# Kernel tuning notes

Hardware: AMD Instinct MI355X
Metric: run time of the kernel (lower is better)

The kernel has to match this reference:

```python
import math
import jax, jax.numpy as jnp
import numpy as np

B, S, E, H = 2, 2048, 1024, 16
Dh = E // H  # 64
ROPE_BASE = 10000.0


def setup_inputs() -> dict:
    key = jax.random.key(0)
    ks = jax.random.split(key, 7)
    f32 = jnp.float32
    return {
        "q": jax.random.normal(ks[0], (B, S, E), dtype=f32),
        "k": jax.random.normal(ks[1], (B, S, E), dtype=f32),
        "v": jax.random.normal(ks[2], (B, S, E), dtype=f32),
        # nn.Linear weights stored torch-style as [out_features, in_features]
        "W_q": jax.random.normal(ks[3], (E, E), dtype=f32) * 0.02,
        "W_k": jax.random.normal(ks[4], (E, E), dtype=f32) * 0.02,
        "W_v": jax.random.normal(ks[5], (E, E), dtype=f32) * 0.02,
        "W_o": jax.random.normal(ks[6], (E, E), dtype=f32) * 0.02,
    }


def _rope(x):
    # x: [B, H, S, Dh]; interleaved-pair rotary embedding along the seq axis.
    d = x.shape[-1]
    pos = jnp.arange(x.shape[2], dtype=x.dtype)
    inv_freq = 1.0 / (ROPE_BASE ** (jnp.arange(0, d, 2, dtype=x.dtype) / d))
    ang = pos[:, None] * inv_freq            # [S, Dh//2]
    cos, sin = jnp.cos(ang), jnp.sin(ang)    # broadcast over [B, H]
    xe, xo = x[..., 0::2], x[..., 1::2]      # even/odd interleaved pairs
    out = jnp.stack([xe * cos - xo * sin, xo * cos + xe * sin], axis=-1)
    return out.reshape(x.shape)


def reference(q, k, v, W_q, W_k, W_v, W_o):
    b, s, e = q.shape
    scale = 1.0 / math.sqrt(e)  # NOTE: 1/sqrt(hidden_dim), not head_dim (faithful)
    # project and split heads: [B, H, S, Dh]
    qh = (q @ W_q.T).reshape(b, s, H, Dh).transpose(0, 2, 1, 3)
    kh = (k @ W_k.T).reshape(b, s, H, Dh).transpose(0, 2, 1, 3)
    vh = (v @ W_v.T).reshape(b, s, H, Dh).transpose(0, 2, 1, 3)
    qh = _rope(qh)
    kh = _rope(kh)
    scores = jnp.einsum('bhsd,bhtd->bhst', qh, kh) * scale
    # Faithful quirk: the original sets causal_mask[0,0] = False, which zeroes
    # the ENTIRE [S,S] mask (dims 0,1 are singletons) -> masked_fill is a no-op.
    probs = jax.nn.softmax(scores, axis=-1)
    out = jnp.einsum('bhst,bhtd->bhsd', probs, vh)
    out = out.transpose(0, 2, 1, 3).reshape(b, s, e)
    return out @ W_o.T
```

## Files before the change

kernel.cpp:

```cpp
#include <hip/hip_runtime.h>
#include <math.h>

#define Bsz 2
#define Ssz 2048
#define Esz 1024
#define Hn  16
#define Dd  64
#define PADC 72

typedef unsigned short ushort_t;
typedef short bf16x8 __attribute__((ext_vector_type(8)));
typedef float f32x4 __attribute__((ext_vector_type(4)));

#define GLD16(g, l) __builtin_amdgcn_global_load_lds(                        \
    (const __attribute__((address_space(1))) unsigned int*)(g),              \
    (__attribute__((address_space(3))) unsigned int*)(l), 16, 0, 0)

__global__ __launch_bounds__(256) void rope_table_kernel(float* tc, float* ts)
{
    const int idx = blockIdx.x * 256 + threadIdx.x;
    const int s = idx >> 5, p = idx & 31;
    const double c = 9.210340371976184257 / 32.0;
    const double inv = exp(-c * (double)p);
    double sn, cs;
    sincos((double)s * inv, &sn, &cs);
    tc[idx] = (float)cs;
    ts[idx] = (float)sn;
}

__device__ inline ushort_t bf16_rn(float x)
{
    unsigned u = __float_as_uint(x);
    return (ushort_t)((u + 0x7FFFu + ((u >> 16) & 1u)) >> 16);
}

__device__ inline void bsplit(float x, ushort_t& h, ushort_t& l)
{
    unsigned u = __float_as_uint(x);
    unsigned hr = (u + 0x7FFFu + ((u >> 16) & 1u)) >> 16;
    h = (ushort_t)hr;
    float lo = x - __uint_as_float(hr << 16);
    l = bf16_rn(lo);
}

__global__ __launch_bounds__(256) void cvt_kernel(
    const float* s0, const float* s1, const float* s2,
    const float* s3, const float* s4, const float* s5,
    ushort_t* d0, ushort_t* d1, ushort_t* d2,
    ushort_t* d3, ushort_t* d4, ushort_t* d5, int n_big, int n_small)
{
    const float* s; ushort_t* d;
    switch (blockIdx.z) {
        case 0: s = s0; d = d0; break;
        case 1: s = s1; d = d1; break;
        case 2: s = s2; d = d2; break;
        case 3: s = s3; d = d3; break;
        case 4: s = s4; d = d4; break;
        default: s = s5; d = d5; break;
    }
    const int n = (blockIdx.z < 3) ? n_big : n_small;
    const int i = (blockIdx.x * 256 + threadIdx.x) * 4;
    if (i >= n) return;
    float4 v = *(const float4*)(s + i);
    ushort4 o;
    o.x = bf16_rn(v.x); o.y = bf16_rn(v.y);
    o.z = bf16_rn(v.z); o.w = bf16_rn(v.w);
    *(ushort4*)(d + i) = o;
}

__global__ __launch_bounds__(256) void wsplit_kernel(
    const float* s, ushort_t* ph, ushort_t* pl, int n)
{
    const int i = (blockIdx.x * 256 + threadIdx.x) * 4;
    if (i >= n) return;
    float4 v = *(const float4*)(s + i);
    ushort4 hv, lv;
    bsplit(v.x, hv.x, lv.x);
    bsplit(v.y, hv.y, lv.y);
    bsplit(v.z, hv.z, lv.z);
    bsplit(v.w, hv.w, lv.w);
    *(ushort4*)(ph + i) = hv;
    *(ushort4*)(pl + i) = lv;
}

__global__ __launch_bounds__(256) void proj_gemm_kernel(
    const ushort_t* __restrict__ Aq, const ushort_t* __restrict__ Ak,
    const ushort_t* __restrict__ Av,
    const ushort_t* __restrict__ Wq, const ushort_t* __restrict__ Wk,
    const ushort_t* __restrict__ Wv,
    ushort_t* __restrict__ Yq, ushort_t* __restrict__ Yk,
    ushort_t* __restrict__ Yv,
    const float* __restrict__ tc, const float* __restrict__ ts)
{
    const int z = blockIdx.z;
    const ushort_t* Ag = (z == 0) ? Aq : (z == 1) ? Ak : Av;
    const ushort_t* Wg = (z == 0) ? Wq : (z == 1) ? Wk : Wv;
    ushort_t*       Yg = (z == 0) ? Yq : (z == 1) ? Yk : Yv;
    const bool rope = (z < 2);

    __shared__ __align__(16) ushort_t sA[128 * 32];
    __shared__ __align__(16) ushort_t sB[64 * 32];

    const int t    = threadIdx.x;
    const int lane = t & 63;
    const int wv   = t >> 6;
    const int wm   = (wv & 1) * 64;
    const int wn   = (wv >> 1) * 32;
    const int fr   = lane & 15;
    const int kq   = (lane >> 4) * 8;
    const int n0   = blockIdx.x * 64;
    const int m0   = blockIdx.y * 128;

    const ushort_t* pA = Ag + (size_t)(m0 + (t >> 2)) * 1024 + (t & 3) * 8;
    const ushort_t* pB = Wg + (size_t)(n0 + (t >> 2)) * 1024 + (t & 3) * 8;

    f32x4 acc[4][2];
#pragma unroll
    for (int mi = 0; mi < 4; ++mi)
#pragma unroll
        for (int ni = 0; ni < 2; ++ni) acc[mi][ni] = (f32x4)0.f;

    for (int k0 = 0; k0 < 1024; k0 += 32) {
        GLD16(pA + k0,             &sA[t * 8]);
        GLD16(pA + k0 + 64 * 1024, &sA[2048 + t * 8]);
        GLD16(pB + k0,             &sB[t * 8]);
        __syncthreads();

        bf16x8 a[4], b[2];
#pragma unroll
        for (int mi = 0; mi < 4; ++mi)
            a[mi] = *(const bf16x8*)&sA[(wm + mi * 16 + fr) * 32 + kq];
#pragma unroll
        for (int ni = 0; ni < 2; ++ni)
            b[ni] = *(const bf16x8*)&sB[(wn + ni * 16 + fr) * 32 + kq];
#pragma unroll
        for (int mi = 0; mi < 4; ++mi)
#pragma unroll
            for (int ni = 0; ni < 2; ++ni)
                acc[mi][ni] = __builtin_amdgcn_mfma_f32_16x16x32_bf16(
                    a[mi], b[ni], acc[mi][ni], 0, 0, 0);
        __syncthreads();
    }

#pragma unroll
    for (int mi = 0; mi < 4; ++mi)
#pragma unroll
        for (int ni = 0; ni < 2; ++ni) {
            const int col   = n0 + wn + ni * 16 + fr;
            const int rbase = m0 + wm + mi * 16 + (lane >> 4) * 4;
            const int hh = col >> 6, d = col & 63, pi = d >> 1;
#pragma unroll
            for (int rg = 0; rg < 4; ++rg) {
                const int srow = rbase + rg;
                const int b_ = srow >> 11, s = srow & (Ssz - 1);
                float v  = acc[mi][ni][rg];
                float pt = __shfl_xor(v, 1, 64);
                float o  = v;
                if (rope) {
                    const float cs = tc[s * 32 + pi];
                    const float sn = ts[s * 32 + pi];
                    o = (d & 1) ? fmaf(v, cs, pt * sn)
                                : fmaf(v, cs, -pt * sn);
                }
                const size_t idx = (z == 2)
                    ? (((size_t)(b_ * Hn + hh)) * Dd + d) * Ssz + s
                    : (((size_t)(b_ * Hn + hh)) * Ssz + s) * Dd + d;
                Yg[idx] = bf16_rn(o);
            }
        }
}

__global__ __launch_bounds__(256) void attn_bf16_kernel(
    const ushort_t* __restrict__ Qb, const ushort_t* __restrict__ Kb,
    const ushort_t* __restrict__ Vtb,
    ushort_t* __restrict__ Oh, ushort_t* __restrict__ Ol)
{
    __shared__ __align__(16) ushort_t sK[64 * PADC];
    __shared__ __align__(16) ushort_t sV[64 * PADC];
    __shared__ __align__(16) ushort_t sP[64 * PADC];

    const int t    = threadIdx.x;
    const int lane = t & 63;
    const int w    = t >> 6;
    const int fr   = lane & 15;
    const int g    = lane >> 4;
    const int kq   = g * 8;
    const int bh   = blockIdx.y;
    const int q0   = blockIdx.x * 64;

    const size_t qbase = ((size_t)bh * Ssz + q0 + w * 16 + fr) * Dd;
    bf16x8 qa[2];
    qa[0] = *(const bf16x8*)(Qb + qbase + kq);
    qa[1] = *(const bf16x8*)(Qb + qbase + 32 + kq);

    float lp[4];
    f32x4 Oacc[4];
#pragma unroll
    for (int r = 0; r < 4; ++r) lp[r] = 0.f;
#pragma unroll
    for (int dt = 0; dt < 4; ++dt) Oacc[dt] = (f32x4)0.f;

    const int srow = t >> 3;
    const int scol = (t & 7) * 8;
    const size_t kgb = (size_t)bh * Ssz * Dd;
    const size_t vgb = (size_t)bh * Dd * Ssz;

    const float kf = 0.045084220027780106f;

    for (int kv0 = 0; kv0 < Ssz; kv0 += 64) {
#pragma unroll
        for (int rr = 0; rr < 2; ++rr) {
            const int row = srow + rr * 32;
            *(uint4*)&sK[row * PADC + scol] =
                *(const uint4*)(Kb + kgb + (size_t)(kv0 + row) * Dd + scol);
            *(uint4*)&sV[row * PADC + scol] =
                *(const uint4*)(Vtb + vgb + (size_t)row * Ssz + kv0 + scol);
        }
        __syncthreads();

        f32x4 S[4];
#pragma unroll
        for (int nt = 0; nt < 4; ++nt) S[nt] = (f32x4)0.f;
#pragma unroll
        for (int ks = 0; ks < 2; ++ks)
#pragma unroll
            for (int nt = 0; nt < 4; ++nt) {
                bf16x8 kf_ = *(const bf16x8*)&sK[(nt * 16 + fr) * PADC + ks * 32 + kq];
                S[nt] = __builtin_amdgcn_mfma_f32_16x16x32_bf16(qa[ks], kf_, S[nt], 0, 0, 0);
            }

#pragma unroll
        for (int nt = 0; nt < 4; ++nt)
#pragma unroll
            for (int rg = 0; rg < 4; ++rg) {
                const float p = exp2f(S[nt][rg] * kf);
                lp[rg] += p;
                sP[(w * 16 + g * 4 + rg) * PADC + nt * 16 + fr] = bf16_rn(p);
            }
        __syncthreads();

#pragma unroll
        for (int ks = 0; ks < 2; ++ks) {
            bf16x8 pa = *(const bf16x8*)&sP[(w * 16 + fr) * PADC + ks * 32 + kq];
#pragma unroll
            for (int dt = 0; dt < 4; ++dt) {
                bf16x8 vf = *(const bf16x8*)&sV[(dt * 16 + fr) * PADC + ks * 32 + kq];
                Oacc[dt] = __builtin_amdgcn_mfma_f32_16x16x32_bf16(pa, vf, Oacc[dt], 0, 0, 0);
            }
        }
        __syncthreads();
    }

#pragma unroll
    for (int rg = 0; rg < 4; ++rg) {
#pragma unroll
        for (int mk = 1; mk <= 8; mk <<= 1)
            lp[rg] += __shfl_xor(lp[rg], mk, 64);
    }

    const int b = bh >> 4, h = bh & 15;
#pragma unroll
    for (int rg = 0; rg < 4; ++rg) {
        const int s = q0 + w * 16 + g * 4 + rg;
        const float inv = 1.f / lp[rg];
#pragma unroll
        for (int dt = 0; dt < 4; ++dt) {
            const float o = Oacc[dt][rg] * inv;
            ushort_t oh, ol;
            bsplit(o, oh, ol);
            const size_t idx = ((size_t)(b * Ssz + s)) * Esz + h * Dd + dt * 16 + fr;
            Oh[idx] = oh;
            Ol[idx] = ol;
        }
    }
}

__global__ __launch_bounds__(256) void final_gemm_kernel(
    const ushort_t* __restrict__ Ahg, const ushort_t* __restrict__ Alg,
    const ushort_t* __restrict__ Bhg, const ushort_t* __restrict__ Blg,
    float* __restrict__ Yf)
{
    __shared__ __align__(16) ushort_t sAh[128 * 32];
    __shared__ __align__(16) ushort_t sAl[128 * 32];
    __shared__ __align__(16) ushort_t sBh[64 * 32];
    __shared__ __align__(16) ushort_t sBl[64 * 32];

    const int t    = threadIdx.x;
    const int lane = t & 63;
    const int wv   = t >> 6;
    const int wm   = (wv & 1) * 64;
    const int wn   = (wv >> 1) * 32;
    const int fr   = lane & 15;
    const int kq   = (lane >> 4) * 8;
    const int n0   = blockIdx.x * 64;
    const int m0   = blockIdx.y * 128;

    const ushort_t* pAh = Ahg + (size_t)(m0 + (t >> 2)) * 1024 + (t & 3) * 8;
    const ushort_t* pAl = Alg + (size_t)(m0 + (t >> 2)) * 1024 + (t & 3) * 8;
    const ushort_t* pBh = Bhg + (size_t)(n0 + (t >> 2)) * 1024 + (t & 3) * 8;
    const ushort_t* pBl = Blg + (size_t)(n0 + (t >> 2)) * 1024 + (t & 3) * 8;

    f32x4 acc[4][2];
#pragma unroll
    for (int mi = 0; mi < 4; ++mi)
#pragma unroll
        for (int ni = 0; ni < 2; ++ni) acc[mi][ni] = (f32x4)0.f;

    for (int k0 = 0; k0 < 1024; k0 += 32) {
        GLD16(pAh + k0,             &sAh[t * 8]);
        GLD16(pAh + k0 + 64 * 1024, &sAh[2048 + t * 8]);
        GLD16(pAl + k0,             &sAl[t * 8]);
        GLD16(pAl + k0 + 64 * 1024, &sAl[2048 + t * 8]);
        GLD16(pBh + k0,             &sBh[t * 8]);
        GLD16(pBl + k0,             &sBl[t * 8]);
        __syncthreads();

        bf16x8 ah[4], al[4], bh[2], bl[2];
#pragma unroll
        for (int mi = 0; mi < 4; ++mi) {
            ah[mi] = *(const bf16x8*)&sAh[(wm + mi * 16 + fr) * 32 + kq];
            al[mi] = *(const bf16x8*)&sAl[(wm + mi * 16 + fr) * 32 + kq];
        }
#pragma unroll
        for (int ni = 0; ni < 2; ++ni) {
            bh[ni] = *(const bf16x8*)&sBh[(wn + ni * 16 + fr) * 32 + kq];
            bl[ni] = *(const bf16x8*)&sBl[(wn + ni * 16 + fr) * 32 + kq];
        }
#pragma unroll
        for (int mi = 0; mi < 4; ++mi)
#pragma unroll
            for (int ni = 0; ni < 2; ++ni) {
                acc[mi][ni] = __builtin_amdgcn_mfma_f32_16x16x32_bf16(
                    ah[mi], bh[ni], acc[mi][ni], 0, 0, 0);
                acc[mi][ni] = __builtin_amdgcn_mfma_f32_16x16x32_bf16(
                    ah[mi], bl[ni], acc[mi][ni], 0, 0, 0);
                acc[mi][ni] = __builtin_amdgcn_mfma_f32_16x16x32_bf16(
                    al[mi], bh[ni], acc[mi][ni], 0, 0, 0);
            }
        __syncthreads();
    }

#pragma unroll
    for (int mi = 0; mi < 4; ++mi)
#pragma unroll
        for (int ni = 0; ni < 2; ++ni) {
            const int col   = n0 + wn + ni * 16 + fr;
            const int rbase = m0 + wm + mi * 16 + (lane >> 4) * 4;
#pragma unroll
            for (int rg = 0; rg < 4; ++rg)
                Yf[(size_t)(rbase + rg) * 1024 + col] = acc[mi][ni][rg];
        }
}

extern "C" void kernel_launch(void* const* d_in, const int* in_sizes, int n_in,
                              void* d_out, int out_size, void* d_ws, size_t ws_size,
                              hipStream_t stream)
{
    (void)in_sizes; (void)n_in; (void)out_size; (void)ws_size;
    const float* q   = (const float*)d_in[0];
    const float* k   = (const float*)d_in[1];
    const float* v   = (const float*)d_in[2];
    const float* W_q = (const float*)d_in[3];
    const float* W_k = (const float*)d_in[4];
    const float* W_v = (const float*)d_in[5];
    const float* W_o = (const float*)d_in[6];
    float* out = (float*)d_out;

    const size_t NQ = (size_t)Bsz * Ssz * Esz;
    const size_t NW = (size_t)Esz * Esz;

    float* ws = (float*)d_ws;
    float* tc = ws;
    float* ts = ws + 65536;

    ushort_t* us  = (ushort_t*)(ws + 131072);
    ushort_t* qb  = us;
    ushort_t* kb  = qb + NQ;
    ushort_t* vb  = kb + NQ;
    ushort_t* wqb = vb + NQ;
    ushort_t* wkb = wqb + NW;
    ushort_t* wvb = wkb + NW;
    ushort_t* woh = wvb + NW;
    ushort_t* wol = woh + NW;
    ushort_t* pq  = wol + NW;
    ushort_t* pk  = pq + NQ;
    ushort_t* pv  = pk + NQ;
    ushort_t* oh  = pv + NQ;
    ushort_t* ol  = oh + NQ;

    dim3 blk(256);

    rope_table_kernel<<<dim3(256), blk, 0, stream>>>(tc, ts);

    cvt_kernel<<<dim3(4096, 1, 6), blk, 0, stream>>>(
        q, k, v, W_q, W_k, W_v, qb, kb, vb, wqb, wkb, wvb, (int)NQ, (int)NW);
    wsplit_kernel<<<dim3(1024), blk, 0, stream>>>(W_o, woh, wol, (int)NW);

    proj_gemm_kernel<<<dim3(Esz / 64, (Bsz * Ssz) / 128, 3), blk, 0, stream>>>(
        qb, kb, vb, wqb, wkb, wvb, pq, pk, pv, tc, ts);

    attn_bf16_kernel<<<dim3(Ssz / 64, Bsz * Hn), blk, 0, stream>>>(
        pq, pk, pv, oh, ol);

    final_gemm_kernel<<<dim3(Esz / 64, (Bsz * Ssz) / 128), blk, 0, stream>>>(
        oh, ol, woh, wol, out);
}
```

Measured before the change: 308.7 us.

## Drop split-bf16 output GEMM, enlarge GEMM/attention tiles, fold softmax scale into Q

The final projection previously used a hi/lo bf16 split (three MFMAs per tile); now both the attention output and W_o are plain bf16 with one MFMA per tile, and the separate weight-split kernel is folded into the conversion kernel. Both GEMMs now use 128x128 tiles, and the attention kernel processes 128 queries per block with two M-tiles per wave, reusing K/V fragments, plus an XOR-swizzled P layout. The softmax scale is folded into Q at projection time, and P is truncated rather than rounded to bf16. This cuts MFMA work and memory traffic at the cost of lower output precision and fewer blocks in the grids.

```diff
diff --git a/kernel.cpp b/kernel.cpp
--- a/kernel.cpp
+++ b/kernel.cpp
@@ -15,6 +15,8 @@
 #define GLD16(g, l) __builtin_amdgcn_global_load_lds(                        \
     (const __attribute__((address_space(1))) unsigned int*)(g),              \
     (__attribute__((address_space(3))) unsigned int*)(l), 16, 0, 0)
+
+#define KF 0.045084220027780106f
 
 __global__ __launch_bounds__(256) void rope_table_kernel(float* tc, float* ts)
 {
@@ -34,20 +36,11 @@
     return (ushort_t)((u + 0x7FFFu + ((u >> 16) & 1u)) >> 16);
 }
 
-__device__ inline void bsplit(float x, ushort_t& h, ushort_t& l)
-{
-    unsigned u = __float_as_uint(x);
-    unsigned hr = (u + 0x7FFFu + ((u >> 16) & 1u)) >> 16;
-    h = (ushort_t)hr;
-    float lo = x - __uint_as_float(hr << 16);
-    l = bf16_rn(lo);
-}
-
 __global__ __launch_bounds__(256) void cvt_kernel(
-    const float* s0, const float* s1, const float* s2,
-    const float* s3, const float* s4, const float* s5,
-    ushort_t* d0, ushort_t* d1, ushort_t* d2,
-    ushort_t* d3, ushort_t* d4, ushort_t* d5, int n_big, int n_small)
+    const float* s0, const float* s1, const float* s2, const float* s3,
+    const float* s4, const float* s5, const float* s6,
+    ushort_t* d0, ushort_t* d1, ushort_t* d2, ushort_t* d3,
+    ushort_t* d4, ushort_t* d5, ushort_t* d6, int n_big, int n_small)
 {
     const float* s; ushort_t* d;
     switch (blockIdx.z) {
@@ -56,7 +49,8 @@
         case 2: s = s2; d = d2; break;
         case 3: s = s3; d = d3; break;
         case 4: s = s4; d = d4; break;
-        default: s = s5; d = d5; break;
+        case 5: s = s5; d = d5; break;
+        default: s = s6; d = d6; break;
     }
     const int n = (blockIdx.z < 3) ? n_big : n_small;
     const int i = (blockIdx.x * 256 + threadIdx.x) * 4;
@@ -68,21 +62,6 @@
     *(ushort4*)(d + i) = o;
 }
 
-__global__ __launch_bounds__(256) void wsplit_kernel(
-    const float* s, ushort_t* ph, ushort_t* pl, int n)
-{
-    const int i = (blockIdx.x * 256 + threadIdx.x) * 4;
-    if (i >= n) return;
-    float4 v = *(const float4*)(s + i);
-    ushort4 hv, lv;
-    bsplit(v.x, hv.x, lv.x);
-    bsplit(v.y, hv.y, lv.y);
-    bsplit(v.z, hv.z, lv.z);
-    bsplit(v.w, hv.w, lv.w);
-    *(ushort4*)(ph + i) = hv;
-    *(ushort4*)(pl + i) = lv;
-}
-
 __global__ __launch_bounds__(256) void proj_gemm_kernel(
     const ushort_t* __restrict__ Aq, const ushort_t* __restrict__ Ak,
     const ushort_t* __restrict__ Av,
@@ -96,47 +75,48 @@
     const ushort_t* Ag = (z == 0) ? Aq : (z == 1) ? Ak : Av;
     const ushort_t* Wg = (z == 0) ? Wq : (z == 1) ? Wk : Wv;
     ushort_t*       Yg = (z == 0) ? Yq : (z == 1) ? Yk : Yv;
-    const bool rope = (z < 2);
 
     __shared__ __align__(16) ushort_t sA[128 * 32];
-    __shared__ __align__(16) ushort_t sB[64 * 32];
+    __shared__ __align__(16) ushort_t sB[128 * 32];
 
     const int t    = threadIdx.x;
     const int lane = t & 63;
-    const int wv   = t >> 6;
-    const int wm   = (wv & 1) * 64;
-    const int wn   = (wv >> 1) * 32;
+    const int w    = t >> 6;
+    const int wm   = (w & 1) * 64;
+    const int wn   = (w >> 1) * 64;
     const int fr   = lane & 15;
-    const int kq   = (lane >> 4) * 8;
-    const int n0   = blockIdx.x * 64;
+    const int g    = lane >> 4;
+    const int kq   = g * 8;
+    const int n0   = blockIdx.x * 128;
     const int m0   = blockIdx.y * 128;
 
     const ushort_t* pA = Ag + (size_t)(m0 + (t >> 2)) * 1024 + (t & 3) * 8;
     const ushort_t* pB = Wg + (size_t)(n0 + (t >> 2)) * 1024 + (t & 3) * 8;
 
-    f32x4 acc[4][2];
+    f32x4 acc[4][4];
 #pragma unroll
     for (int mi = 0; mi < 4; ++mi)
 #pragma unroll
-        for (int ni = 0; ni < 2; ++ni) acc[mi][ni] = (f32x4)0.f;
+        for (int ni = 0; ni < 4; ++ni) acc[mi][ni] = (f32x4)0.f;
 
     for (int k0 = 0; k0 < 1024; k0 += 32) {
         GLD16(pA + k0,             &sA[t * 8]);
         GLD16(pA + k0 + 64 * 1024, &sA[2048 + t * 8]);
         GLD16(pB + k0,             &sB[t * 8]);
-        __syncthreads();
-
-        bf16x8 a[4], b[2];
+        GLD16(pB + k0 + 64 * 1024, &sB[2048 + t * 8]);
+        __syncthreads();
+
+        bf16x8 a[4], b[4];
 #pragma unroll
         for (int mi = 0; mi < 4; ++mi)
             a[mi] = *(const bf16x8*)&sA[(wm + mi * 16 + fr) * 32 + kq];
 #pragma unroll
-        for (int ni = 0; ni < 2; ++ni)
+        for (int ni = 0; ni < 4; ++ni)
             b[ni] = *(const bf16x8*)&sB[(wn + ni * 16 + fr) * 32 + kq];
 #pragma unroll
         for (int mi = 0; mi < 4; ++mi)
 #pragma unroll
-            for (int ni = 0; ni < 2; ++ni)
+            for (int ni = 0; ni < 4; ++ni)
                 acc[mi][ni] = __builtin_amdgcn_mfma_f32_16x16x32_bf16(
                     a[mi], b[ni], acc[mi][ni], 0, 0, 0);
         __syncthreads();
@@ -145,9 +125,9 @@
 #pragma unroll
     for (int mi = 0; mi < 4; ++mi)
 #pragma unroll
-        for (int ni = 0; ni < 2; ++ni) {
+        for (int ni = 0; ni < 4; ++ni) {
             const int col   = n0 + wn + ni * 16 + fr;
-            const int rbase = m0 + wm + mi * 16 + (lane >> 4) * 4;
+            const int rbase = m0 + wm + mi * 16 + g * 4;
             const int hh = col >> 6, d = col & 63, pi = d >> 1;
 #pragma unroll
             for (int rg = 0; rg < 4; ++rg) {
@@ -156,11 +136,12 @@
                 float v  = acc[mi][ni][rg];
                 float pt = __shfl_xor(v, 1, 64);
                 float o  = v;
-                if (rope) {
+                if (z < 2) {
                     const float cs = tc[s * 32 + pi];
                     const float sn = ts[s * 32 + pi];
                     o = (d & 1) ? fmaf(v, cs, pt * sn)
                                 : fmaf(v, cs, -pt * sn);
+                    if (z == 0) o *= KF;
                 }
                 const size_t idx = (z == 2)
                     ? (((size_t)(b_ * Hn + hh)) * Dd + d) * Ssz + s
@@ -170,14 +151,13 @@
         }
 }
 
-__global__ __launch_bounds__(256) void attn_bf16_kernel(
+__global__ __launch_bounds__(256) void attn_kernel(
     const ushort_t* __restrict__ Qb, const ushort_t* __restrict__ Kb,
-    const ushort_t* __restrict__ Vtb,
-    ushort_t* __restrict__ Oh, ushort_t* __restrict__ Ol)
+    const ushort_t* __restrict__ Vtb, ushort_t* __restrict__ Ob)
 {
     __shared__ __align__(16) ushort_t sK[64 * PADC];
     __shared__ __align__(16) ushort_t sV[64 * PADC];
-    __shared__ __align__(16) ushort_t sP[64 * PADC];
+    __shared__ __align__(16) ushort_t sP[128 * PADC];
 
     const int t    = threadIdx.x;
     const int lane = t & 63;
@@ -186,26 +166,42 @@
     const int g    = lane >> 4;
     const int kq   = g * 8;
     const int bh   = blockIdx.y;
-    const int q0   = blockIdx.x * 64;
-
-    const size_t qbase = ((size_t)bh * Ssz + q0 + w * 16 + fr) * Dd;
-    bf16x8 qa[2];
-    qa[0] = *(const bf16x8*)(Qb + qbase + kq);
-    qa[1] = *(const bf16x8*)(Qb + qbase + 32 + kq);
-
-    float lp[4];
-    f32x4 Oacc[4];
-#pragma unroll
-    for (int r = 0; r < 4; ++r) lp[r] = 0.f;
-#pragma unroll
-    for (int dt = 0; dt < 4; ++dt) Oacc[dt] = (f32x4)0.f;
+    const int q0   = blockIdx.x * 128;
+
+    const int frh = fr >> 3;
+    const int frl = fr & 7;
+    const int fq  = (fr >> 2) & 3;
+
+    int scolP[4], krdP[2];
+#pragma unroll
+    for (int nt = 0; nt < 4; ++nt)
+        scolP[nt] = (((nt * 2 + frh) ^ g) << 3) + frl;
+#pragma unroll
+    for (int ks = 0; ks < 2; ++ks)
+        krdP[ks] = ((4 * ks + g) ^ fq) << 3;
+
+    bf16x8 qa[2][2];
+#pragma unroll
+    for (int mt = 0; mt < 2; ++mt) {
+        const size_t qbase = ((size_t)bh * Ssz + q0 + w * 32 + mt * 16 + fr) * Dd;
+        qa[mt][0] = *(const bf16x8*)(Qb + qbase + kq);
+        qa[mt][1] = *(const bf16x8*)(Qb + qbase + 32 + kq);
+    }
+
+    float lp[2][4];
+    f32x4 Oacc[2][4];
+#pragma unroll
+    for (int mt = 0; mt < 2; ++mt) {
+#pragma unroll
+        for (int rg = 0; rg < 4; ++rg) lp[mt][rg] = 0.f;
+#pragma unroll
+        for (int dt = 0; dt < 4; ++dt) Oacc[mt][dt] = (f32x4)0.f;
+    }
 
     const int srow = t >> 3;
     const int scol = (t & 7) * 8;
     const size_t kgb = (size_t)bh * Ssz * Dd;
     const size_t vgb = (size_t)bh * Dd * Ssz;
-
-    const float kf = 0.045084220027780106f;
 
     for (int kv0 = 0; kv0 < Ssz; kv0 += 64) {
 #pragma unroll
@@ -218,134 +214,133 @@
         }
         __syncthreads();
 
-        f32x4 S[4];
-#pragma unroll
-        for (int nt = 0; nt < 4; ++nt) S[nt] = (f32x4)0.f;
+        f32x4 S[2][4];
+#pragma unroll
+        for (int mt = 0; mt < 2; ++mt)
+#pragma unroll
+            for (int nt = 0; nt < 4; ++nt) S[mt][nt] = (f32x4)0.f;
 #pragma unroll
         for (int ks = 0; ks < 2; ++ks)
 #pragma unroll
             for (int nt = 0; nt < 4; ++nt) {
-                bf16x8 kf_ = *(const bf16x8*)&sK[(nt * 16 + fr) * PADC + ks * 32 + kq];
-                S[nt] = __builtin_amdgcn_mfma_f32_16x16x32_bf16(qa[ks], kf_, S[nt], 0, 0, 0);
+                bf16x8 kfrag = *(const bf16x8*)&sK[(nt * 16 + fr) * PADC + ks * 32 + kq];
+#pragma unroll
+                for (int mt = 0; mt < 2; ++mt)
+                    S[mt][nt] = __builtin_amdgcn_mfma_f32_16x16x32_bf16(
+                        qa[mt][ks], kfrag, S[mt][nt], 0, 0, 0);
             }
 
 #pragma unroll
-        for (int nt = 0; nt < 4; ++nt)
-#pragma unroll
-            for (int rg = 0; rg < 4; ++rg) {
-                const float p = exp2f(S[nt][rg] * kf);
-                lp[rg] += p;
-                sP[(w * 16 + g * 4 + rg) * PADC + nt * 16 + fr] = bf16_rn(p);
+        for (int mt = 0; mt < 2; ++mt)
+#pragma unroll
+            for (int nt = 0; nt < 4; ++nt)
+#pragma unroll
+                for (int rg = 0; rg < 4; ++rg) {
+                    const float p = exp2f(S[mt][nt][rg]);
+                    lp[mt][rg] += p;
+                    sP[(w * 32 + mt * 16 + g * 4 + rg) * PADC + scolP[nt]] =
+                        (ushort_t)(__float_as_uint(p) >> 16);
+                }
+        __syncthreads();
+
+#pragma unroll
+        for (int ks = 0; ks < 2; ++ks) {
+            bf16x8 pa[2];
+#pragma unroll
+            for (int mt = 0; mt < 2; ++mt)
+                pa[mt] = *(const bf16x8*)&sP[(w * 32 + mt * 16 + fr) * PADC + krdP[ks]];
+#pragma unroll
+            for (int dt = 0; dt < 4; ++dt) {
+                bf16x8 vfrag = *(const bf16x8*)&sV[(dt * 16 + fr) * PADC + ks * 32 + kq];
+#pragma unroll
+                for (int mt = 0; mt < 2; ++mt)
+                    Oacc[mt][dt] = __builtin_amdgcn_mfma_f32_16x16x32_bf16(
+                        pa[mt], vfrag, Oacc[mt][dt], 0, 0, 0);
             }
-        __syncthreads();
-
-#pragma unroll
-        for (int ks = 0; ks < 2; ++ks) {
-            bf16x8 pa = *(const bf16x8*)&sP[(w * 16 + fr) * PADC + ks * 32 + kq];
+        }
+        __syncthreads();
+    }
+
+#pragma unroll
+    for (int mt = 0; mt < 2; ++mt)
+#pragma unroll
+        for (int rg = 0; rg < 4; ++rg) {
+#pragma unroll
+            for (int mk = 1; mk <= 8; mk <<= 1)
+                lp[mt][rg] += __shfl_xor(lp[mt][rg], mk, 64);
+        }
+
+    const int b = bh >> 4, h = bh & 15;
+#pragma unroll
+    for (int mt = 0; mt < 2; ++mt)
+#pragma unroll
+        for (int rg = 0; rg < 4; ++rg) {
+            const int s = q0 + w * 32 + mt * 16 + g * 4 + rg;
+            const float inv = 1.f / lp[mt][rg];
 #pragma unroll
             for (int dt = 0; dt < 4; ++dt) {
-                bf16x8 vf = *(const bf16x8*)&sV[(dt * 16 + fr) * PADC + ks * 32 + kq];
-                Oacc[dt] = __builtin_amdgcn_mfma_f32_16x16x32_bf16(pa, vf, Oacc[dt], 0, 0, 0);
+                const float o = Oacc[mt][dt][rg] * inv;
+                Ob[((size_t)(b * Ssz + s)) * Esz + h * Dd + dt * 16 + fr] = bf16_rn(o);
             }
         }
-        __syncthreads();
-    }
-
-#pragma unroll
-    for (int rg = 0; rg < 4; ++rg) {
-#pragma unroll
-        for (int mk = 1; mk <= 8; mk <<= 1)
-            lp[rg] += __shfl_xor(lp[rg], mk, 64);
-    }
-
-    const int b = bh >> 4, h = bh & 15;
-#pragma unroll
-    for (int rg = 0; rg < 4; ++rg) {
-        const int s = q0 + w * 16 + g * 4 + rg;
-        const float inv = 1.f / lp[rg];
-#pragma unroll
-        for (int dt = 0; dt < 4; ++dt) {
-            const float o = Oacc[dt][rg] * inv;
-            ushort_t oh, ol;
-            bsplit(o, oh, ol);
-            const size_t idx = ((size_t)(b * Ssz + s)) * Esz + h * Dd + dt * 16 + fr;
-            Oh[idx] = oh;
-            Ol[idx] = ol;
-        }
-    }
 }
 
 __global__ __launch_bounds__(256) void final_gemm_kernel(
-    const ushort_t* __restrict__ Ahg, const ushort_t* __restrict__ Alg,
-    const ushort_t* __restrict__ Bhg, const ushort_t* __restrict__ Blg,
+    const ushort_t* __restrict__ Ag, const ushort_t* __restrict__ Bg,
     float* __restrict__ Yf)
 {
-    __shared__ __align__(16) ushort_t sAh[128 * 32];
-    __shared__ __align__(16) ushort_t sAl[128 * 32];
-    __shared__ __align__(16) ushort_t sBh[64 * 32];
-    __shared__ __align__(16) ushort_t sBl[64 * 32];
+    __shared__ __align__(16) ushort_t sA[128 * 32];
+    __shared__ __align__(16) ushort_t sB[128 * 32];
 
     const int t    = threadIdx.x;
     const int lane = t & 63;
-    const int wv   = t >> 6;
-    const int wm   = (wv & 1) * 64;
-    const int wn   = (wv >> 1) * 32;
+    const int w    = t >> 6;
+    const int wm   = (w & 1) * 64;
+    const int wn   = (w >> 1) * 64;
     const int fr   = lane & 15;
-    const int kq   = (lane >> 4) * 8;
-    const int n0   = blockIdx.x * 64;
+    const int g    = lane >> 4;
+    const int kq   = g * 8;
+    const int n0   = blockIdx.x * 128;
     const int m0   = blockIdx.y * 128;
 
-    const ushort_t* pAh = Ahg + (size_t)(m0 + (t >> 2)) * 1024 + (t & 3) * 8;
-    const ushort_t* pAl = Alg + (size_t)(m0 + (t >> 2)) * 1024 + (t & 3) * 8;
-    const ushort_t* pBh = Bhg + (size_t)(n0 + (t >> 2)) * 1024 + (t & 3) * 8;
-    const ushort_t* pBl = Blg + (size_t)(n0 + (t >> 2)) * 1024 + (t & 3) * 8;
-
-    f32x4 acc[4][2];
+    const ushort_t* pA = Ag + (size_t)(m0 + (t >> 2)) * 1024 + (t & 3) * 8;
+    const ushort_t* pB = Bg + (size_t)(n0 + (t >> 2)) * 1024 + (t & 3) * 8;
+
+    f32x4 acc[4][4];
 #pragma unroll
     for (int mi = 0; mi < 4; ++mi)
 #pragma unroll
-        for (int ni = 0; ni < 2; ++ni) acc[mi][ni] = (f32x4)0.f;
+        for (int ni = 0; ni < 4; ++ni) acc[mi][ni] = (f32x4)0.f;
 
     for (int k0 = 0; k0 < 1024; k0 += 32) {
-        GLD16(pAh + k0,             &sAh[t * 8]);
-        GLD16(pAh + k0 + 64 * 1024, &sAh[2048 + t * 8]);
-        GLD16(pAl + k0,             &sAl[t * 8]);
-        GLD16(pAl + k0 + 64 * 1024, &sAl[2048 + t * 8]);
-        GLD16(pBh + k0,             &sBh[t * 8]);
-        GLD16(pBl + k0,             &sBl[t * 8]);
-        __syncthreads();
-
-        bf16x8 ah[4], al[4], bh[2], bl[2];
-#pragma unroll
-        for (int mi = 0; mi < 4; ++mi) {
-            ah[mi] = *(const bf16x8*)&sAh[(wm + mi * 16 + fr) * 32 + kq];
-            al[mi] = *(const bf16x8*)&sAl[(wm + mi * 16 + fr) * 32 + kq];
-        }
-#pragma unroll
-        for (int ni = 0; ni < 2; ++ni) {
-            bh[ni] = *(const bf16x8*)&sBh[(wn + ni * 16 + fr) * 32 + kq];
-            bl[ni] = *(const bf16x8*)&sBl[(wn + ni * 16 + fr) * 32 + kq];
-        }
+        GLD16(pA + k0,             &sA[t * 8]);
+        GLD16(pA + k0 + 64 * 1024, &sA[2048 + t * 8]);
+        GLD16(pB + k0,             &sB[t * 8]);
+        GLD16(pB + k0 + 64 * 1024, &sB[2048 + t * 8]);
+        __syncthreads();
+
+        bf16x8 a[4], b[4];
 #pragma unroll
         for (int mi = 0; mi < 4; ++mi)
-#pragma unroll
-            for (int ni = 0; ni < 2; ++ni) {
+            a[mi] = *(const bf16x8*)&sA[(wm + mi * 16 + fr) * 32 + kq];
+#pragma unroll
+        for (int ni = 0; ni < 4; ++ni)
+            b[ni] = *(const bf16x8*)&sB[(wn + ni * 16 + fr) * 32 + kq];
+#pragma unroll
+        for (int mi = 0; mi < 4; ++mi)
+#pragma unroll
+            for (int ni = 0; ni < 4; ++ni)
                 acc[mi][ni] = __builtin_amdgcn_mfma_f32_16x16x32_bf16(
-                    ah[mi], bh[ni], acc[mi][ni], 0, 0, 0);
-                acc[mi][ni] = __builtin_amdgcn_mfma_f32_16x16x32_bf16(
-                    ah[mi], bl[ni], acc[mi][ni], 0, 0, 0);
-                acc[mi][ni] = __builtin_amdgcn_mfma_f32_16x16x32_bf16(
-                    al[mi], bh[ni], acc[mi][ni], 0, 0, 0);
-            }
+                    a[mi], b[ni], acc[mi][ni], 0, 0, 0);
         __syncthreads();
     }
 
 #pragma unroll
     for (int mi = 0; mi < 4; ++mi)
 #pragma unroll
-        for (int ni = 0; ni < 2; ++ni) {
+        for (int ni = 0; ni < 4; ++ni) {
             const int col   = n0 + wn + ni * 16 + fr;
-            const int rbase = m0 + wm + mi * 16 + (lane >> 4) * 4;
+            const int rbase = m0 + wm + mi * 16 + g * 4;
 #pragma unroll
             for (int rg = 0; rg < 4; ++rg)
                 Yf[(size_t)(rbase + rg) * 1024 + col] = acc[mi][ni][rg];
@@ -380,28 +375,25 @@
     ushort_t* wqb = vb + NQ;
     ushort_t* wkb = wqb + NW;
     ushort_t* wvb = wkb + NW;
-    ushort_t* woh = wvb + NW;
-    ushort_t* wol = woh + NW;
-    ushort_t* pq  = wol + NW;
+    ushort_t* wob = wvb + NW;
+    ushort_t* pq  = wob + NW;
     ushort_t* pk  = pq + NQ;
     ushort_t* pv  = pk + NQ;
-    ushort_t* oh  = pv + NQ;
-    ushort_t* ol  = oh + NQ;
+    ushort_t* ob  = pv + NQ;
 
     dim3 blk(256);
 
     rope_table_kernel<<<dim3(256), blk, 0, stream>>>(tc, ts);
 
-    cvt_kernel<<<dim3(4096, 1, 6), blk, 0, stream>>>(
-        q, k, v, W_q, W_k, W_v, qb, kb, vb, wqb, wkb, wvb, (int)NQ, (int)NW);
-    wsplit_kernel<<<dim3(1024), blk, 0, stream>>>(W_o, woh, wol, (int)NW);
-
-    proj_gemm_kernel<<<dim3(Esz / 64, (Bsz * Ssz) / 128, 3), blk, 0, stream>>>(
+    cvt_kernel<<<dim3(4096, 1, 7), blk, 0, stream>>>(
+        q, k, v, W_q, W_k, W_v, W_o,
+        qb, kb, vb, wqb, wkb, wvb, wob, (int)NQ, (int)NW);
+
+    proj_gemm_kernel<<<dim3(Esz / 128, (Bsz * Ssz) / 128, 3), blk, 0, stream>>>(
         qb, kb, vb, wqb, wkb, wvb, pq, pk, pv, tc, ts);
 
-    attn_bf16_kernel<<<dim3(Ssz / 64, Bsz * Hn), blk, 0, stream>>>(
-        pq, pk, pv, oh, ol);
-
-    final_gemm_kernel<<<dim3(Esz / 64, (Bsz * Ssz) / 128), blk, 0, stream>>>(
-        oh, ol, woh, wol, out);
-}
+    attn_kernel<<<dim3(Ssz / 128, Bsz * Hn), blk, 0, stream>>>(pq, pk, pv, ob);
+
+    final_gemm_kernel<<<dim3(Esz / 128, (Bsz * Ssz) / 128), blk, 0, stream>>>(
+        ob, wob, out);
+}
```

After: 312.1 us. No clear change (+1.1%).
